# Kernel optimization log

Hardware: AMD Instinct MI355X
Metric: run time of the kernel (lower is better)

The kernel has to match this reference:

```python
import jax, jax.numpy as jnp
import numpy as np

D_MODEL = 1024
NUM_HEADS = 16
THETA = 10000.0


def _rope(x, positions):
    # x: [..., S, d_k] with interleaved even/odd pairs; positions: [S] int
    d_k = x.shape[-1]
    inv_freq = 1.0 / (THETA ** (jnp.arange(0, d_k, 2, dtype=jnp.float32) / d_k))  # [d_k/2]
    freqs = positions.astype(jnp.float32)[:, None] * inv_freq[None, :]  # [S, d_k/2]
    cos = jnp.cos(freqs)
    sin = jnp.sin(freqs)
    x_even = x[..., 0::2]
    x_odd = x[..., 1::2]
    rot_even = x_even * cos - x_odd * sin
    rot_odd = x_even * sin + x_odd * cos
    out = jnp.stack([rot_even, rot_odd], axis=-1)  # [..., S, d_k/2, 2]
    return out.reshape(x.shape)


def setup_inputs() -> dict:
    key = jax.random.key(0)
    k1, k2, k3 = jax.random.split(key, 3)
    B, S = 2, 2048
    x = jax.random.normal(k1, (B, S, D_MODEL), dtype=jnp.float32)
    Wqkv = jax.random.normal(k2, (3 * D_MODEL, D_MODEL), dtype=jnp.float32) * (D_MODEL ** -0.5)
    Wout = jax.random.normal(k3, (D_MODEL, D_MODEL), dtype=jnp.float32) * (D_MODEL ** -0.5)
    token_positions = jnp.arange(S, dtype=jnp.int32)
    return {"x": x, "Wqkv": Wqkv, "Wout": Wout, "token_positions": token_positions}


def reference(x, Wqkv, Wout, token_positions):
    B, S, D = x.shape
    H = NUM_HEADS
    d_k = D // H
    qkv = x @ Wqkv.T  # [B, S, 3D]
    qkv = qkv.reshape(B, S, 3, H, d_k).transpose(0, 2, 3, 1, 4)  # [B, 3, H, S, d_k]
    q, k, v = qkv[:, 0], qkv[:, 1], qkv[:, 2]  # each [B, H, S, d_k]
    q = _rope(q, token_positions)
    k = _rope(k, token_positions)
    scores = jnp.einsum("bhqd,bhkd->bhqk", q, k) / jnp.sqrt(jnp.float32(d_k))
    attn = jax.nn.softmax(scores, axis=-1)
    out = jnp.einsum("bhqk,bhkd->bhqd", attn, v)  # [B, H, S, d_k]
    out = out.transpose(0, 2, 1, 3).reshape(B, S, D)
    return out @ Wout.T
```

## Files before the change

### kernel.cpp

```cpp
#include <hip/hip_runtime.h>
#include <stdint.h>

typedef unsigned short u16;
typedef unsigned int u32;
typedef __bf16 bf16x8 __attribute__((ext_vector_type(8)));
typedef float f32x4 __attribute__((ext_vector_type(4)));

#define MFMA16 __builtin_amdgcn_mfma_f32_16x16x32_bf16

static __device__ __forceinline__ u16 f2bf(float f) {
  union { float f; u32 u; } v; v.f = f;
  u32 r = v.u + 0x7FFFu + ((v.u >> 16) & 1u);
  return (u16)(r >> 16);
}
static __device__ __forceinline__ float bf2f(u16 b) {
  union { float f; u32 u; } v; v.u = ((u32)b) << 16;
  return v.f;
}
static __device__ __forceinline__ void load_lds16(const void* g, void* l) {
  __builtin_amdgcn_global_load_lds(
      (const __attribute__((address_space(1))) void*)g,
      (__attribute__((address_space(3))) void*)l, 16, 0, 0);
}

__global__ __launch_bounds__(256) void cvt_bf16(const float* __restrict__ in,
                                                u16* __restrict__ out, int n4) {
  int i = blockIdx.x * 256 + threadIdx.x;
  if (i >= n4) return;
  float4 v = reinterpret_cast<const float4*>(in)[i];
  uint2 r;
  r.x = (u32)f2bf(v.x) | ((u32)f2bf(v.y) << 16);
  r.y = (u32)f2bf(v.z) | ((u32)f2bf(v.w) << 16);
  reinterpret_cast<uint2*>(out)[i] = r;
}

template <bool OUT_BF16>
__global__ __launch_bounds__(256, 2) void gemm_bt(const u16* __restrict__ A,
                                                  const u16* __restrict__ B,
                                                  void* __restrict__ Cv,
                                                  int M, int N, int K) {
  __shared__ u16 As[128 * 32];
  __shared__ u16 Bs[128 * 32];
  const int t = threadIdx.x;
  const int w = t >> 6, lane = t & 63;
  const int brow = blockIdx.y * 128, bcol = blockIdx.x * 128;
  const int wr = (w >> 1) * 64, wc = (w & 1) * 64;

  f32x4 acc[4][4];
#pragma unroll
  for (int i = 0; i < 4; ++i)
#pragma unroll
    for (int j = 0; j < 4; ++j) acc[i][j] = (f32x4){0.f, 0.f, 0.f, 0.f};

  const int srow = w * 16 + (lane >> 2);
  const int scol = (lane & 3) * 8;
  const u16* ga = A + (size_t)(brow + srow) * K + scol;
  const u16* gb = B + (size_t)(bcol + srow) * K + scol;
  const size_t rstep = (size_t)64 * K;
  u16* ldsA = As + w * 512;
  u16* ldsB = Bs + w * 512;

  const int lc = lane & 15, lg = lane >> 4;
  const int kg = lg * 8;

  const int nk = K >> 5;
  for (int kt = 0; kt < nk; ++kt) {
    __syncthreads();
    load_lds16(ga, ldsA);
    load_lds16(ga + rstep, (char*)ldsA + 4096);
    load_lds16(gb, ldsB);
    load_lds16(gb + rstep, (char*)ldsB + 4096);
    ga += 32; gb += 32;
    asm volatile("s_waitcnt vmcnt(0)" ::: "memory");
    __syncthreads();
    bf16x8 af[4], bfr[4];
#pragma unroll
    for (int i = 0; i < 4; ++i)
      af[i] = *reinterpret_cast<const bf16x8*>(As + (wr + i * 16 + lc) * 32 + kg);
#pragma unroll
    for (int j = 0; j < 4; ++j)
      bfr[j] = *reinterpret_cast<const bf16x8*>(Bs + (wc + j * 16 + lc) * 32 + kg);
#pragma unroll
    for (int i = 0; i < 4; ++i)
#pragma unroll
      for (int j = 0; j < 4; ++j)
        acc[i][j] = MFMA16(af[i], bfr[j], acc[i][j], 0, 0, 0);
  }

  const int r0 = lg * 4;
#pragma unroll
  for (int i = 0; i < 4; ++i)
#pragma unroll
    for (int j = 0; j < 4; ++j)
#pragma unroll
      for (int r = 0; r < 4; ++r) {
        const int m = brow + wr + i * 16 + r0 + r;
        const int n = bcol + wc + j * 16 + lc;
        if constexpr (OUT_BF16)
          ((u16*)Cv)[(size_t)m * N + n] = f2bf(acc[i][j][r]);
        else
          ((float*)Cv)[(size_t)m * N + n] = acc[i][j][r];
      }
}

__global__ __launch_bounds__(256) void build_trig(const int* __restrict__ pos,
                                                  float2* __restrict__ tab) {
  int i = blockIdx.x * 256 + threadIdx.x;
  int s = i >> 5, p = i & 31;
  float inv = powf(10000.0f, -(float)p * (1.0f / 32.0f));
  float fr = (float)pos[s] * inv;
  float sn, cs;
  sincosf(fr, &sn, &cs);
  tab[i] = make_float2(cs, sn);
}

__global__ __launch_bounds__(256) void rope_repack(const u16* __restrict__ qkv,
                                                   const float2* __restrict__ tab,
                                                   u16* __restrict__ Qro,
                                                   u16* __restrict__ Kro) {
  int idx = blockIdx.x * 256 + threadIdx.x;
  int p = idx & 31;
  int h = (idx >> 5) & 15;
  int m = idx >> 9;
  int b = m >> 11, s = m & 2047;
  const u32* row = reinterpret_cast<const u32*>(qkv + (size_t)m * 3072);
  u32 qp = row[h * 32 + p];
  u32 kp = row[512 + h * 32 + p];
  float2 cssn = tab[s * 32 + p];
  float cs = cssn.x, sn = cssn.y;
  float qe = bf2f((u16)(qp & 0xffffu)), qo = bf2f((u16)(qp >> 16));
  float ke = bf2f((u16)(kp & 0xffffu)), ko = bf2f((u16)(kp >> 16));
  float qre = (qe * cs - qo * sn) * 0.125f;
  float qro_ = (qe * sn + qo * cs) * 0.125f;
  float kre = ke * cs - ko * sn;
  float kro_ = ke * sn + ko * cs;
  size_t o = ((size_t)(b * 16 + h) * 2048 + s) * 32 + p;
  reinterpret_cast<u32*>(Qro)[o] = (u32)f2bf(qre) | ((u32)f2bf(qro_) << 16);
  reinterpret_cast<u32*>(Kro)[o] = (u32)f2bf(kre) | ((u32)f2bf(kro_) << 16);
}

__global__ __launch_bounds__(256) void v_transpose(const u16* __restrict__ qkv,
                                                   u16* __restrict__ VT) {
  const int bh = blockIdx.y;
  const int s0 = blockIdx.x * 64;
  const int b = bh >> 4, h = bh & 15;
  __shared__ u16 tile[64][72];
  const int t = threadIdx.x;
#pragma unroll
  for (int c = 0; c < 2; ++c) {
    int r = c * 32 + (t >> 3);
    int d = (t & 7) * 8;
    const u16* src = qkv + (size_t)(b * 2048 + s0 + r) * 3072 + 2048 + h * 64 + d;
    *reinterpret_cast<uint4*>(&tile[r][d]) = *reinterpret_cast<const uint4*>(src);
  }
  __syncthreads();
#pragma unroll
  for (int c = 0; c < 2; ++c) {
    int dd = c * 32 + (t >> 3);
    int sg = (t & 7) * 8;
    u16 tmp[8];
#pragma unroll
    for (int jj = 0; jj < 8; ++jj) tmp[jj] = tile[sg + jj][dd];
    *reinterpret_cast<uint4*>(VT + ((size_t)bh * 64 + dd) * 2048 + s0 + sg) =
        *reinterpret_cast<const uint4*>(tmp);
  }
}

__global__ __launch_bounds__(256, 2) void attn_fwd(const u16* __restrict__ Q,
                                                   const u16* __restrict__ Kg,
                                                   const u16* __restrict__ VTg,
                                                   u16* __restrict__ O) {
  constexpr int S = 2048;
  __shared__ u16 Kl[64 * 64];
  __shared__ u16 Vl[64 * 64];
  __shared__ u16 Pl[4][32 * 64];
  const int t = threadIdx.x, w = t >> 6, lane = t & 63;
  const int bh = blockIdx.y;
  const int q0 = blockIdx.x * 128 + w * 32;
  const size_t base = (size_t)bh * S * 64;
  const int lc = lane & 15, lg = lane >> 4;

  bf16x8 qf[2][2];
#pragma unroll
  for (int i = 0; i < 2; ++i)
#pragma unroll
    for (int ks = 0; ks < 2; ++ks)
      qf[i][ks] = *reinterpret_cast<const bf16x8*>(
          Q + base + (size_t)(q0 + i * 16 + lc) * 64 + ks * 32 + lg * 8);

  f32x4 Oa[2][4];
  float mrow[2][4], lsum[2][4];
#pragma unroll
  for (int i = 0; i < 2; ++i) {
#pragma unroll
    for (int j = 0; j < 4; ++j) Oa[i][j] = (f32x4){0.f, 0.f, 0.f, 0.f};
#pragma unroll
    for (int r = 0; r < 4; ++r) { mrow[i][r] = -__builtin_inff(); lsum[i][r] = 0.f; }
  }

  u16* Pw = Pl[w];
  for (int kt = 0; kt < S / 64; ++kt) {
    __syncthreads();
#pragma unroll
    for (int c = 0; c < 2; ++c) {
      const int o = c * 4096 + w * 1024 + lane * 16;
      const int row = o >> 7;
      const int swz = (o & 127) ^ ((row & 7) << 4);
      load_lds16((const char*)(Kg + base + kt * 4096) + row * 128 + swz,
                 (char*)Kl + c * 4096 + w * 1024);
      load_lds16((const char*)(VTg + base) + (size_t)row * (S * 2) + kt * 128 + swz,
                 (char*)Vl + c * 4096 + w * 1024);
    }
    asm volatile("s_waitcnt vmcnt(0)" ::: "memory");
    __syncthreads();

    f32x4 Sa[2][4];
#pragma unroll
    for (int i = 0; i < 2; ++i)
#pragma unroll
      for (int j = 0; j < 4; ++j) Sa[i][j] = (f32x4){0.f, 0.f, 0.f, 0.f};
#pragma unroll
    for (int ks = 0; ks < 2; ++ks) {
      bf16x8 kf[4];
#pragma unroll
      for (int j = 0; j < 4; ++j) {
        int kv = j * 16 + lc;
        int a = (kv * 128 + ks * 64 + lg * 16) ^ ((kv & 7) << 4);
        kf[j] = *reinterpret_cast<const bf16x8*>((const char*)Kl + a);
      }
#pragma unroll
      for (int i = 0; i < 2; ++i)
#pragma unroll
        for (int j = 0; j < 4; ++j)
          Sa[i][j] = MFMA16(qf[i][ks], kf[j], Sa[i][j], 0, 0, 0);
    }

    float pm[2][4];
#pragma unroll
    for (int i = 0; i < 2; ++i)
#pragma unroll
      for (int r = 0; r < 4; ++r)
        pm[i][r] = fmaxf(fmaxf(Sa[i][0][r], Sa[i][1][r]),
                         fmaxf(Sa[i][2][r], Sa[i][3][r]));
#pragma unroll
    for (int msk = 1; msk < 16; msk <<= 1)
#pragma unroll
      for (int i = 0; i < 2; ++i)
#pragma unroll
        for (int r = 0; r < 4; ++r)
          pm[i][r] = fmaxf(pm[i][r], __shfl_xor(pm[i][r], msk));

    float sc[2][4];
#pragma unroll
    for (int i = 0; i < 2; ++i)
#pragma unroll
      for (int r = 0; r < 4; ++r) {
        float mn = fmaxf(mrow[i][r], pm[i][r]);
        sc[i][r] = __expf(mrow[i][r] - mn);
        mrow[i][r] = mn;
      }

    float pv[2][4][4];
    float rs[2][4];
#pragma unroll
    for (int i = 0; i < 2; ++i)
#pragma unroll
      for (int r = 0; r < 4; ++r) rs[i][r] = 0.f;
#pragma unroll
    for (int i = 0; i < 2; ++i)
#pragma unroll
      for (int j = 0; j < 4; ++j)
#pragma unroll
        for (int r = 0; r < 4; ++r) {
          float e = __expf(Sa[i][j][r] - mrow[i][r]);
          pv[i][j][r] = e;
          rs[i][r] += e;
        }
#pragma unroll
    for (int msk = 1; msk < 16; msk <<= 1)
#pragma unroll
      for (int i = 0; i < 2; ++i)
#pragma unroll
        for (int r = 0; r < 4; ++r)
          rs[i][r] += __shfl_xor(rs[i][r], msk);
#pragma unroll
    for (int i = 0; i < 2; ++i)
#pragma unroll
      for (int r = 0; r < 4; ++r)
        lsum[i][r] = lsum[i][r] * sc[i][r] + rs[i][r];
#pragma unroll
    for (int i = 0; i < 2; ++i)
#pragma unroll
      for (int j = 0; j < 4; ++j)
#pragma unroll
        for (int r = 0; r < 4; ++r) Oa[i][j][r] *= sc[i][r];

#pragma unroll
    for (int i = 0; i < 2; ++i)
#pragma unroll
      for (int j = 0; j < 4; ++j)
#pragma unroll
        for (int r = 0; r < 4; ++r) {
          int qloc = i * 16 + lg * 4 + r;
          int kv = j * 16 + lc;
          int a = (qloc * 128 + kv * 2) ^ ((qloc & 7) << 4);
          *(u16*)((char*)Pw + a) = f2bf(pv[i][j][r]);
        }
    asm volatile("s_waitcnt lgkmcnt(0)" ::: "memory");
    __builtin_amdgcn_sched_barrier(0);

#pragma unroll
    for (int ks = 0; ks < 2; ++ks) {
      bf16x8 pa[2], vf[4];
#pragma unroll
      for (int i = 0; i < 2; ++i) {
        int qloc = i * 16 + lc;
        int a = (qloc * 128 + ks * 64 + lg * 16) ^ ((qloc & 7) << 4);
        pa[i] = *reinterpret_cast<const bf16x8*>((const char*)Pw + a);
      }
#pragma unroll
      for (int j = 0; j < 4; ++j) {
        int d = j * 16 + lc;
        int a = (d * 128 + ks * 64 + lg * 16) ^ ((d & 7) << 4);
        vf[j] = *reinterpret_cast<const bf16x8*>((const char*)Vl + a);
      }
#pragma unroll
      for (int i = 0; i < 2; ++i)
#pragma unroll
        for (int j = 0; j < 4; ++j)
          Oa[i][j] = MFMA16(pa[i], vf[j], Oa[i][j], 0, 0, 0);
    }
  }

  const int b = bh >> 4, h = bh & 15;
#pragma unroll
  for (int i = 0; i < 2; ++i)
#pragma unroll
    for (int j = 0; j < 4; ++j)
#pragma unroll
      for (int r = 0; r < 4; ++r) {
        int s = q0 + i * 16 + lg * 4 + r;
        float v = Oa[i][j][r] / lsum[i][r];
        O[(size_t)(b * S + s) * 1024 + h * 64 + j * 16 + lc] = f2bf(v);
      }
}

extern "C" void kernel_launch(void* const* d_in, const int* in_sizes, int n_in,
                              void* d_out, int out_size, void* d_ws, size_t ws_size,
                              hipStream_t stream) {
  (void)in_sizes; (void)n_in; (void)out_size; (void)ws_size;
  const float* x = (const float*)d_in[0];
  const float* wqkv = (const float*)d_in[1];
  const float* wout = (const float*)d_in[2];
  const int* pos = (const int*)d_in[3];
  float* out = (float*)d_out;

  char* ws = (char*)d_ws;
  u16* xb     = (u16*)(ws);
  u16* wqkvb  = (u16*)(ws + 8388608);
  u16* woutb  = (u16*)(ws + 14680064);
  u16* qkvb   = (u16*)(ws + 16777216);
  u16* qro    = (u16*)(ws + 41943040);
  u16* kro    = (u16*)(ws + 50331648);
  u16* vt     = (u16*)(ws + 58720256);
  u16* attno  = (u16*)(ws + 67108864);
  float2* tab = (float2*)(ws + 75497472);

  cvt_bf16<<<4096, 256, 0, stream>>>(x, xb, 1048576);
  cvt_bf16<<<3072, 256, 0, stream>>>(wqkv, wqkvb, 786432);
  cvt_bf16<<<1024, 256, 0, stream>>>(wout, woutb, 262144);
  build_trig<<<256, 256, 0, stream>>>(pos, tab);
  gemm_bt<true><<<dim3(24, 32), 256, 0, stream>>>(xb, wqkvb, qkvb, 4096, 3072, 1024);
  rope_repack<<<8192, 256, 0, stream>>>(qkvb, tab, qro, kro);
  v_transpose<<<dim3(32, 32), 256, 0, stream>>>(qkvb, vt);
  attn_fwd<<<dim3(16, 32), 256, 0, stream>>>(qro, kro, vt, attno);
  gemm_bt<false><<<dim3(8, 32), 256, 0, stream>>>(attno, woutb, out, 4096, 1024, 1024);
}
```

Measured before the change: 255.5 us.

## Rewrite attention with 32x32 MFMA, register-resident P, and triple-buffered K/V

Replaces the attention kernel with one built on 32x32x16 bf16 MFMA, computing S^T so each lane owns one query row. The P fragments are converted and exchanged across lanes with cvt_pk and permlane32_swap instead of a round-trip through LDS. K/V tiles are triple-buffered with async global-to-LDS loads so loads overlap compute, and log2(e) is folded into the Q scale so the kernel can use exp2. Rescaling is skipped unless the running max grows by more than a threshold, and blocks are remapped for locality. The cost is more complex synchronisation and a lazy-rescale approximation that relies on the value range staying bounded.

```diff
diff --git a/kernel.cpp b/kernel.cpp
--- a/kernel.cpp
+++ b/kernel.cpp
@@ -5,8 +5,10 @@
 typedef unsigned int u32;
 typedef __bf16 bf16x8 __attribute__((ext_vector_type(8)));
 typedef float f32x4 __attribute__((ext_vector_type(4)));
+typedef float f32x16 __attribute__((ext_vector_type(16)));
 
 #define MFMA16 __builtin_amdgcn_mfma_f32_16x16x32_bf16
+#define MFMA32 __builtin_amdgcn_mfma_f32_32x32x16_bf16
 
 static __device__ __forceinline__ u16 f2bf(float f) {
   union { float f; u32 u; } v; v.f = f;
@@ -130,8 +132,9 @@
   float cs = cssn.x, sn = cssn.y;
   float qe = bf2f((u16)(qp & 0xffffu)), qo = bf2f((u16)(qp >> 16));
   float ke = bf2f((u16)(kp & 0xffffu)), ko = bf2f((u16)(kp >> 16));
-  float qre = (qe * cs - qo * sn) * 0.125f;
-  float qro_ = (qe * sn + qo * cs) * 0.125f;
+  const float QS = 0.18033688011112042f;
+  float qre = (qe * cs - qo * sn) * QS;
+  float qro_ = (qe * sn + qo * cs) * QS;
   float kre = ke * cs - ko * sn;
   float kro_ = ke * sn + ko * cs;
   size_t o = ((size_t)(b * 16 + h) * 2048 + s) * 32 + p;
@@ -166,183 +169,168 @@
   }
 }
 
-__global__ __launch_bounds__(256, 2) void attn_fwd(const u16* __restrict__ Q,
-                                                   const u16* __restrict__ Kg,
-                                                   const u16* __restrict__ VTg,
-                                                   u16* __restrict__ O) {
-  constexpr int S = 2048;
-  __shared__ u16 Kl[64 * 64];
-  __shared__ u16 Vl[64 * 64];
-  __shared__ u16 Pl[4][32 * 64];
-  const int t = threadIdx.x, w = t >> 6, lane = t & 63;
-  const int bh = blockIdx.y;
-  const int q0 = blockIdx.x * 128 + w * 32;
-  const size_t base = (size_t)bh * S * 64;
-  const int lc = lane & 15, lg = lane >> 4;
-
-  bf16x8 qf[2][2];
+__global__ __launch_bounds__(256) void attn_fwd2(const u16* __restrict__ Q,
+                                                 const u16* __restrict__ Kg,
+                                                 const u16* __restrict__ VTg,
+                                                 u16* __restrict__ O) {
+  constexpr int S = 2048, NT = 32;
+  __shared__ char lds[3][16384];
+  const int t = threadIdx.x, wv = t >> 6, lane = t & 63;
+  const int bid = blockIdx.x;
+  const int slot = bid >> 3;
+  const int bh = (bid & 7) * 4 + (slot >> 4);
+  const int qb = slot & 15;
+  const int b = bh >> 4, h = bh & 15;
+  const int q0 = qb * 128 + wv * 32;
+  const size_t kbase = (size_t)bh * (S * 64);
+  const int l31 = lane & 31, hi = lane >> 5;
+
+  bf16x8 qf[4];
+  {
+    const u16* qp = Q + kbase + (size_t)(q0 + l31) * 64 + hi * 8;
+#pragma unroll
+    for (int d = 0; d < 4; ++d)
+      qf[d] = *reinterpret_cast<const bf16x8*>(qp + d * 16);
+  }
+
+  f32x16 Oacc[2];
 #pragma unroll
   for (int i = 0; i < 2; ++i)
 #pragma unroll
-    for (int ks = 0; ks < 2; ++ks)
-      qf[i][ks] = *reinterpret_cast<const bf16x8*>(
-          Q + base + (size_t)(q0 + i * 16 + lc) * 64 + ks * 32 + lg * 8);
-
-  f32x4 Oa[2][4];
-  float mrow[2][4], lsum[2][4];
-#pragma unroll
-  for (int i = 0; i < 2; ++i) {
-#pragma unroll
-    for (int j = 0; j < 4; ++j) Oa[i][j] = (f32x4){0.f, 0.f, 0.f, 0.f};
-#pragma unroll
-    for (int r = 0; r < 4; ++r) { mrow[i][r] = -__builtin_inff(); lsum[i][r] = 0.f; }
-  }
-
-  u16* Pw = Pl[w];
-  for (int kt = 0; kt < S / 64; ++kt) {
-    __syncthreads();
-#pragma unroll
-    for (int c = 0; c < 2; ++c) {
-      const int o = c * 4096 + w * 1024 + lane * 16;
-      const int row = o >> 7;
-      const int swz = (o & 127) ^ ((row & 7) << 4);
-      load_lds16((const char*)(Kg + base + kt * 4096) + row * 128 + swz,
-                 (char*)Kl + c * 4096 + w * 1024);
-      load_lds16((const char*)(VTg + base) + (size_t)row * (S * 2) + kt * 128 + swz,
-                 (char*)Vl + c * 4096 + w * 1024);
+    for (int r = 0; r < 16; ++r) Oacc[i][r] = 0.f;
+  float m = -__builtin_inff(), lsum = 0.f;
+
+  const char* gk0 = (const char*)(Kg + kbase);
+  const char* gv0 = (const char*)(VTg + kbase);
+
+#define STAGE(KT, BUF)                                                         \
+  {                                                                            \
+    char* lk_ = lds[BUF];                                                      \
+    const char* gk_ = gk0 + (size_t)(KT) * 8192;                               \
+    _Pragma("unroll") for (int c_ = 0; c_ < 2; ++c_) {                         \
+      int o_ = (c_ * 256 + t) * 16;                                            \
+      int row_ = o_ >> 7, colb_ = o_ & 127;                                    \
+      int swz_ = colb_ ^ ((row_ & 7) << 4);                                    \
+      load_lds16(gk_ + row_ * 128 + swz_, lk_ + o_);                           \
+      load_lds16(gv0 + (size_t)row_ * 4096 + (KT) * 128 + swz_,                \
+                 lk_ + 8192 + o_);                                             \
+    }                                                                          \
+  }
+
+  STAGE(0, 0)
+  STAGE(1, 1)
+  asm volatile("s_waitcnt vmcnt(4)" ::: "memory");
+  __builtin_amdgcn_s_barrier();
+
+  int cur = 0;
+  for (int kt = 0; kt < NT; ++kt) {
+    const int nxt = kt + 2 < NT ? kt + 2 : NT - 1;
+    const int nbuf = cur + 2 >= 3 ? cur - 1 : cur + 2;
+    STAGE(nxt, nbuf)
+    const char* lk = lds[cur];
+    const char* lv = lds[cur] + 8192;
+
+    f32x16 Sa[2];
+#pragma unroll
+    for (int i = 0; i < 2; ++i)
+#pragma unroll
+      for (int r = 0; r < 16; ++r) Sa[i][r] = 0.f;
+#pragma unroll
+    for (int d = 0; d < 4; ++d) {
+#pragma unroll
+      for (int kvt = 0; kvt < 2; ++kvt) {
+        int kv = kvt * 32 + l31;
+        int a = (kv * 128 + d * 32 + hi * 16) ^ ((kv & 7) << 4);
+        bf16x8 kf = *reinterpret_cast<const bf16x8*>(lk + a);
+        Sa[kvt] = MFMA32(kf, qf[d], Sa[kvt], 0, 0, 0);
+      }
     }
-    asm volatile("s_waitcnt vmcnt(0)" ::: "memory");
-    __syncthreads();
-
-    f32x4 Sa[2][4];
-#pragma unroll
-    for (int i = 0; i < 2; ++i)
-#pragma unroll
-      for (int j = 0; j < 4; ++j) Sa[i][j] = (f32x4){0.f, 0.f, 0.f, 0.f};
-#pragma unroll
-    for (int ks = 0; ks < 2; ++ks) {
-      bf16x8 kf[4];
-#pragma unroll
-      for (int j = 0; j < 4; ++j) {
-        int kv = j * 16 + lc;
-        int a = (kv * 128 + ks * 64 + lg * 16) ^ ((kv & 7) << 4);
-        kf[j] = *reinterpret_cast<const bf16x8*>((const char*)Kl + a);
-      }
+
+    float pmax = Sa[0][0];
+#pragma unroll
+    for (int r = 1; r < 16; ++r) pmax = fmaxf(pmax, Sa[0][r]);
+#pragma unroll
+    for (int r = 0; r < 16; ++r) pmax = fmaxf(pmax, Sa[1][r]);
+    pmax = fmaxf(pmax, __shfl_xor(pmax, 32));
+
+    if (__any(pmax > m + 6.0f)) {
+      float mn = fmaxf(m, pmax);
+      float sc = exp2f(m - mn);
+      m = mn;
+      lsum *= sc;
 #pragma unroll
       for (int i = 0; i < 2; ++i)
 #pragma unroll
-        for (int j = 0; j < 4; ++j)
-          Sa[i][j] = MFMA16(qf[i][ks], kf[j], Sa[i][j], 0, 0, 0);
+        for (int r = 0; r < 16; ++r) Oacc[i][r] *= sc;
     }
 
-    float pm[2][4];
-#pragma unroll
-    for (int i = 0; i < 2; ++i)
-#pragma unroll
-      for (int r = 0; r < 4; ++r)
-        pm[i][r] = fmaxf(fmaxf(Sa[i][0][r], Sa[i][1][r]),
-                         fmaxf(Sa[i][2][r], Sa[i][3][r]));
-#pragma unroll
-    for (int msk = 1; msk < 16; msk <<= 1)
-#pragma unroll
-      for (int i = 0; i < 2; ++i)
-#pragma unroll
-        for (int r = 0; r < 4; ++r)
-          pm[i][r] = fmaxf(pm[i][r], __shfl_xor(pm[i][r], msk));
-
-    float sc[2][4];
-#pragma unroll
-    for (int i = 0; i < 2; ++i)
-#pragma unroll
-      for (int r = 0; r < 4; ++r) {
-        float mn = fmaxf(mrow[i][r], pm[i][r]);
-        sc[i][r] = __expf(mrow[i][r] - mn);
-        mrow[i][r] = mn;
-      }
-
-    float pv[2][4][4];
-    float rs[2][4];
-#pragma unroll
-    for (int i = 0; i < 2; ++i)
-#pragma unroll
-      for (int r = 0; r < 4; ++r) rs[i][r] = 0.f;
-#pragma unroll
-    for (int i = 0; i < 2; ++i)
-#pragma unroll
-      for (int j = 0; j < 4; ++j)
-#pragma unroll
-        for (int r = 0; r < 4; ++r) {
-          float e = __expf(Sa[i][j][r] - mrow[i][r]);
-          pv[i][j][r] = e;
-          rs[i][r] += e;
-        }
-#pragma unroll
-    for (int msk = 1; msk < 16; msk <<= 1)
-#pragma unroll
-      for (int i = 0; i < 2; ++i)
-#pragma unroll
-        for (int r = 0; r < 4; ++r)
-          rs[i][r] += __shfl_xor(rs[i][r], msk);
-#pragma unroll
-    for (int i = 0; i < 2; ++i)
-#pragma unroll
-      for (int r = 0; r < 4; ++r)
-        lsum[i][r] = lsum[i][r] * sc[i][r] + rs[i][r];
-#pragma unroll
-    for (int i = 0; i < 2; ++i)
-#pragma unroll
-      for (int j = 0; j < 4; ++j)
-#pragma unroll
-        for (int r = 0; r < 4; ++r) Oa[i][j][r] *= sc[i][r];
-
-#pragma unroll
-    for (int i = 0; i < 2; ++i)
-#pragma unroll
-      for (int j = 0; j < 4; ++j)
-#pragma unroll
-        for (int r = 0; r < 4; ++r) {
-          int qloc = i * 16 + lg * 4 + r;
-          int kv = j * 16 + lc;
-          int a = (qloc * 128 + kv * 2) ^ ((qloc & 7) << 4);
-          *(u16*)((char*)Pw + a) = f2bf(pv[i][j][r]);
-        }
-    asm volatile("s_waitcnt lgkmcnt(0)" ::: "memory");
-    __builtin_amdgcn_sched_barrier(0);
-
-#pragma unroll
-    for (int ks = 0; ks < 2; ++ks) {
-      bf16x8 pa[2], vf[4];
-#pragma unroll
-      for (int i = 0; i < 2; ++i) {
-        int qloc = i * 16 + lc;
-        int a = (qloc * 128 + ks * 64 + lg * 16) ^ ((qloc & 7) << 4);
-        pa[i] = *reinterpret_cast<const bf16x8*>((const char*)Pw + a);
-      }
-#pragma unroll
-      for (int j = 0; j < 4; ++j) {
-        int d = j * 16 + lc;
-        int a = (d * 128 + ks * 64 + lg * 16) ^ ((d & 7) << 4);
-        vf[j] = *reinterpret_cast<const bf16x8*>((const char*)Vl + a);
-      }
-#pragma unroll
-      for (int i = 0; i < 2; ++i)
-#pragma unroll
-        for (int j = 0; j < 4; ++j)
-          Oa[i][j] = MFMA16(pa[i], vf[j], Oa[i][j], 0, 0, 0);
+    float rs = 0.f;
+#pragma unroll
+    for (int kvt = 0; kvt < 2; ++kvt)
+#pragma unroll
+      for (int r = 0; r < 16; ++r) {
+        float p = exp2f(Sa[kvt][r] - m);
+        Sa[kvt][r] = p;
+        rs += p;
+      }
+    rs += __shfl_xor(rs, 32);
+    lsum += rs;
+
+    bf16x8 pfrag[4];
+#pragma unroll
+    for (int kvt = 0; kvt < 2; ++kvt)
+#pragma unroll
+      for (int s1 = 0; s1 < 2; ++s1) {
+        u32 X0, X1, Y0, Y1;
+        const int c0 = s1 * 8, c1 = c0 + 4;
+        asm("v_cvt_pk_bf16_f32 %0, %1, %2"
+            : "=v"(X0) : "v"(Sa[kvt][c0 + 0]), "v"(Sa[kvt][c0 + 1]));
+        asm("v_cvt_pk_bf16_f32 %0, %1, %2"
+            : "=v"(X1) : "v"(Sa[kvt][c0 + 2]), "v"(Sa[kvt][c0 + 3]));
+        asm("v_cvt_pk_bf16_f32 %0, %1, %2"
+            : "=v"(Y0) : "v"(Sa[kvt][c1 + 0]), "v"(Sa[kvt][c1 + 1]));
+        asm("v_cvt_pk_bf16_f32 %0, %1, %2"
+            : "=v"(Y1) : "v"(Sa[kvt][c1 + 2]), "v"(Sa[kvt][c1 + 3]));
+        asm("v_permlane32_swap_b32 %0, %1" : "+v"(X0), "+v"(Y0));
+        asm("v_permlane32_swap_b32 %0, %1" : "+v"(X1), "+v"(Y1));
+        union { u32 w[4]; bf16x8 v; } u;
+        u.w[0] = X0; u.w[1] = X1; u.w[2] = Y0; u.w[3] = Y1;
+        pfrag[kvt * 2 + s1] = u.v;
+      }
+
+#pragma unroll
+    for (int s = 0; s < 4; ++s) {
+#pragma unroll
+      for (int dt = 0; dt < 2; ++dt) {
+        int d = dt * 32 + l31;
+        int a = (d * 128 + s * 32 + hi * 16) ^ ((d & 7) << 4);
+        bf16x8 vf = *reinterpret_cast<const bf16x8*>(lv + a);
+        Oacc[dt] = MFMA32(vf, pfrag[s], Oacc[dt], 0, 0, 0);
+      }
     }
-  }
-
-  const int b = bh >> 4, h = bh & 15;
-#pragma unroll
-  for (int i = 0; i < 2; ++i)
-#pragma unroll
-    for (int j = 0; j < 4; ++j)
-#pragma unroll
-      for (int r = 0; r < 4; ++r) {
-        int s = q0 + i * 16 + lg * 4 + r;
-        float v = Oa[i][j][r] / lsum[i][r];
-        O[(size_t)(b * S + s) * 1024 + h * 64 + j * 16 + lc] = f2bf(v);
-      }
+
+    asm volatile("s_waitcnt vmcnt(4)" ::: "memory");
+    __builtin_amdgcn_s_barrier();
+    cur = cur + 1 == 3 ? 0 : cur + 1;
+  }
+#undef STAGE
+
+  const float rdiv = 1.0f / lsum;
+  const int srow = q0 + l31;
+  u16* orow = O + (size_t)(b * S + srow) * 1024 + h * 64;
+#pragma unroll
+  for (int dt = 0; dt < 2; ++dt)
+#pragma unroll
+    for (int c = 0; c < 4; ++c) {
+      float v0 = Oacc[dt][4 * c + 0] * rdiv;
+      float v1 = Oacc[dt][4 * c + 1] * rdiv;
+      float v2 = Oacc[dt][4 * c + 2] * rdiv;
+      float v3 = Oacc[dt][4 * c + 3] * rdiv;
+      uint2 pk;
+      pk.x = (u32)f2bf(v0) | ((u32)f2bf(v1) << 16);
+      pk.y = (u32)f2bf(v2) | ((u32)f2bf(v3) << 16);
+      *reinterpret_cast<uint2*>(orow + dt * 32 + c * 8 + hi * 4) = pk;
+    }
 }
 
 extern "C" void kernel_launch(void* const* d_in, const int* in_sizes, int n_in,
@@ -373,6 +361,6 @@
   gemm_bt<true><<<dim3(24, 32), 256, 0, stream>>>(xb, wqkvb, qkvb, 4096, 3072, 1024);
   rope_repack<<<8192, 256, 0, stream>>>(qkvb, tab, qro, kro);
   v_transpose<<<dim3(32, 32), 256, 0, stream>>>(qkvb, vt);
-  attn_fwd<<<dim3(16, 32), 256, 0, stream>>>(qro, kro, vt, attno);
+  attn_fwd2<<<512, 256, 0, stream>>>(qro, kro, vt, attno);
   gemm_bt<false><<<dim3(8, 32), 256, 0, stream>>>(attno, woutb, out, 4096, 1024, 1024);
 }
```

After: 231.5 us. -9.4%, faster.
